# Performance work log

Measured on AMD Instinct MI355X. Metric: run time of the kernel, lower is better.

Reference implementation:

```python
import jax, jax.numpy as jnp
import numpy as np


def _sobel_filters():
    # fil is the 3x3 smoothing kernel [[1,2,1],[2,4,2],[1,2,1]]
    fil = np.array([[1, 2, 1], [2, 4, 2], [1, 2, 1]], dtype=np.float32)
    fx = np.zeros((3, 3, 3), dtype=np.float32)
    fx[0, :, :] = fil
    fx[2, :, :] = -fil
    fy = np.zeros((3, 3, 3), dtype=np.float32)
    fy[:, 0, :] = fil
    fy[:, 2, :] = -fil
    fz = np.zeros((3, 3, 3), dtype=np.float32)
    fz[:, :, 0] = fil
    fz[:, :, 2] = -fil
    # Stack the three fixed (non-learned) filters as 3 output channels: [O=3, I=1, 3,3,3]
    return jnp.asarray(np.stack([fx, fy, fz])[:, None])


_FILT = _sobel_filters()
_DN = ('NCDHW', 'OIDHW', 'NCDHW')


def _grad3d(v):
    # v: [N,1,D,H,W] -> [N,3,D,H,W], padding=1 == SAME for 3x3x3 stride 1
    return jax.lax.conv_general_dilated(
        v, _FILT.astype(v.dtype), window_strides=(1, 1, 1),
        padding='SAME', dimension_numbers=_DN)


def setup_inputs() -> dict:
    key = jax.random.key(0)
    k1, k2 = jax.random.split(key)
    shape = (2, 1, 160, 192, 224)
    x = jax.random.normal(k1, shape, dtype=jnp.float32)
    y = jax.random.normal(k2, shape, dtype=jnp.float32)
    return {"x": x, "y": y}


def reference(x, y):
    gx = _grad3d(x)  # [N,3,D,H,W]
    gy = _grad3d(y)
    d2 = (gx - gy) ** 2
    # sum over the 3 directions of the per-direction MSE
    return jnp.sum(jnp.mean(d2, axis=(0, 2, 3, 4)))
```

## Files before the change

### kernel.cpp

```cpp
#include <hip/hip_runtime.h>


#define N_  2
#define D_  160
#define H_  192
#define W_  224
#define PS  (H_ * W_)

#define TD   8
#define WOUT 62

constexpr float SCALE = 1.0f / ((float)N_ * D_ * H_ * W_);

__global__ __launch_bounds__(256, 6)
void grad_loss_kernel(const float* __restrict__ x, const float* __restrict__ y,
                      float* __restrict__ out) {
    __shared__ float wsum[4];

    const int tid  = threadIdx.x;
    const int lane = tid & 63;
    const int wv   = tid >> 6;

    const int w  = blockIdx.x * WOUT + lane - 1;
    const int h0 = blockIdx.y * 16 + wv * 4;
    const int nchunks = D_ / TD;
    const int nb = blockIdx.z / nchunks;
    const int d0 = (blockIdx.z % nchunks) * TD;

    const bool wok    = (unsigned)w < (unsigned)W_;
    const bool active = (lane >= 1) && (lane <= 62) && wok;

    bool hv[6];
    #pragma unroll
    for (int r = 0; r < 6; ++r)
        hv[r] = (unsigned)(h0 - 1 + r) < (unsigned)H_;

    const float* bx = x + (size_t)nb * D_ * PS;
    const float* by = y + (size_t)nb * D_ * PS;
    const int obase = h0 * W_ + w;

    float a0[4], a1[4], a2[4], b0[4], b1[4], b2[4];
    float vc[6];
    float acc = 0.f;

    {
        const int p = d0 - 1;
        const bool pin = p >= 0;
        #pragma unroll
        for (int r = 0; r < 6; ++r) {
            float xv = 0.f, yv = 0.f;
            if (pin && hv[r] && wok) {
                int o = obase + p * PS + (r - 1) * W_;
                xv = bx[o]; yv = by[o];
            }
            vc[r] = xv - yv;
        }
    }

    #pragma unroll
    for (int it = 0; it <= TD + 1; ++it) {
        float xn[6], yn[6];
        const int p = d0 + it;
        const bool pref = (it <= TD) && (p < D_);
        #pragma unroll
        for (int r = 0; r < 6; ++r) {
            xn[r] = 0.f; yn[r] = 0.f;
            if (pref && hv[r] && wok) {
                int o = obase + p * PS + (r - 1) * W_;
                xn[r] = bx[o]; yn[r] = by[o];
            }
        }

        float sw[6], gw[6];
        #pragma unroll
        for (int r = 0; r < 6; ++r) {
            float L  = __shfl_up(vc[r], 1, 64);
            float Rt = __shfl_down(vc[r], 1, 64);
            sw[r] = (L + Rt) + 2.f * vc[r];
            gw[r] = L - Rt;
        }
        float n0[4], n1[4], n2[4];
        #pragma unroll
        for (int j = 0; j < 4; ++j) {
            n0[j] = sw[j] + 2.f * sw[j + 1] + sw[j + 2];
            n1[j] = sw[j] - sw[j + 2];
            n2[j] = gw[j] + 2.f * gw[j + 1] + gw[j + 2];
        }

        if (it >= 2 && active) {
            #pragma unroll
            for (int j = 0; j < 4; ++j) {
                float gx = a0[j] - n0[j];
                float gy = a1[j] + 2.f * b1[j] + n1[j];
                float gz = a2[j] + 2.f * b2[j] + n2[j];
                acc = fmaf(gx, gx, acc);
                acc = fmaf(gy, gy, acc);
                acc = fmaf(gz, gz, acc);
            }
        }

        #pragma unroll
        for (int j = 0; j < 4; ++j) {
            a0[j] = b0[j]; a1[j] = b1[j]; a2[j] = b2[j];
            b0[j] = n0[j]; b1[j] = n1[j]; b2[j] = n2[j];
        }

        #pragma unroll
        for (int r = 0; r < 6; ++r) vc[r] = xn[r] - yn[r];
    }

    #pragma unroll
    for (int off = 32; off > 0; off >>= 1)
        acc += __shfl_xor(acc, off, 64);
    if (lane == 0) wsum[wv] = acc;
    __syncthreads();
    if (tid == 0) {
        float s = (wsum[0] + wsum[1]) + (wsum[2] + wsum[3]);
        atomicAdd(out, s * SCALE);
    }
}

extern "C" void kernel_launch(void* const* d_in, const int* in_sizes, int n_in,
                              void* d_out, int out_size, void* d_ws, size_t ws_size,
                              hipStream_t stream) {
    const float* x = (const float*)d_in[0];
    const float* y = (const float*)d_in[1];
    float* out = (float*)d_out;

    hipMemsetAsync(out, 0, sizeof(float), stream);

    dim3 block(256);
    dim3 grid((W_ + WOUT - 1) / WOUT,
              H_ / 16,
              N_ * (D_ / TD));
    grad_loss_kernel<<<grid, block, 0, stream>>>(x, y, out);
}
```

Before: 149.6 us.

## Vectorize W with float4 per lane and map one H row per wave

Each lane now handles four consecutive W elements through float4 loads, and one wave covers a full 224-wide row, so there are no overlapping halo columns in W and the grid no longer splits W. Each wave processes one H row and still loads the three neighbouring rows, which raises H-halo reloads from 6/4 to 3/1 per output row. The intent is wider, better-coalesced loads and less wasted work at W tile edges. In exchange, 8 of 64 lanes sit idle, register pressure rises (launch bounds lowered to 4), and traffic from redundant H rows goes up.

```diff
diff --git a/kernel.cpp b/kernel.cpp
--- a/kernel.cpp
+++ b/kernel.cpp
@@ -8,11 +8,10 @@
 #define PS  (H_ * W_)
 
 #define TD   8
-#define WOUT 62
 
 constexpr float SCALE = 1.0f / ((float)N_ * D_ * H_ * W_);
 
-__global__ __launch_bounds__(256, 6)
+__global__ __launch_bounds__(256, 4)
 void grad_loss_kernel(const float* __restrict__ x, const float* __restrict__ y,
                       float* __restrict__ out) {
     __shared__ float wsum[4];
@@ -21,92 +20,110 @@
     const int lane = tid & 63;
     const int wv   = tid >> 6;
 
-    const int w  = blockIdx.x * WOUT + lane - 1;
-    const int h0 = blockIdx.y * 16 + wv * 4;
+    const int h  = blockIdx.y * 4 + wv;
     const int nchunks = D_ / TD;
     const int nb = blockIdx.z / nchunks;
     const int d0 = (blockIdx.z % nchunks) * TD;
 
-    const bool wok    = (unsigned)w < (unsigned)W_;
-    const bool active = (lane >= 1) && (lane <= 62) && wok;
+    const bool wact = lane < 56;
+    const int  w0   = lane * 4;
 
-    bool hv[6];
+    const float* bx = x + (size_t)nb * ((size_t)D_ * PS);
+    const float* by = y + (size_t)nb * ((size_t)D_ * PS);
+
+    bool rok[3];
+    int  ro[3];
     #pragma unroll
-    for (int r = 0; r < 6; ++r)
-        hv[r] = (unsigned)(h0 - 1 + r) < (unsigned)H_;
+    for (int r = 0; r < 3; ++r) {
+        int hr = h - 1 + r;
+        rok[r] = ((unsigned)hr < (unsigned)H_) && wact;
+        ro[r]  = hr * W_ + w0;
+    }
 
-    const float* bx = x + (size_t)nb * D_ * PS;
-    const float* by = y + (size_t)nb * D_ * PS;
-    const int obase = h0 * W_ + w;
-
-    float a0[4], a1[4], a2[4], b0[4], b1[4], b2[4];
-    float vc[6];
+    const float4 z4 = make_float4(0.f, 0.f, 0.f, 0.f);
+    float4 vc[3];
+    float4 a0, a1, a2, b0, b1, b2;
     float acc = 0.f;
 
     {
         const int p = d0 - 1;
         const bool pin = p >= 0;
         #pragma unroll
-        for (int r = 0; r < 6; ++r) {
-            float xv = 0.f, yv = 0.f;
-            if (pin && hv[r] && wok) {
-                int o = obase + p * PS + (r - 1) * W_;
-                xv = bx[o]; yv = by[o];
+        for (int r = 0; r < 3; ++r) {
+            vc[r] = z4;
+            if (pin && rok[r]) {
+                const float4 xv = *(const float4*)(bx + p * PS + ro[r]);
+                const float4 yv = *(const float4*)(by + p * PS + ro[r]);
+                vc[r] = make_float4(xv.x - yv.x, xv.y - yv.y,
+                                    xv.z - yv.z, xv.w - yv.w);
             }
-            vc[r] = xv - yv;
         }
     }
 
     #pragma unroll
     for (int it = 0; it <= TD + 1; ++it) {
-        float xn[6], yn[6];
+        float4 xn[3], yn[3];
         const int p = d0 + it;
         const bool pref = (it <= TD) && (p < D_);
         #pragma unroll
-        for (int r = 0; r < 6; ++r) {
-            xn[r] = 0.f; yn[r] = 0.f;
-            if (pref && hv[r] && wok) {
-                int o = obase + p * PS + (r - 1) * W_;
-                xn[r] = bx[o]; yn[r] = by[o];
+        for (int r = 0; r < 3; ++r) {
+            xn[r] = z4; yn[r] = z4;
+            if (pref && rok[r]) {
+                xn[r] = *(const float4*)(bx + p * PS + ro[r]);
+                yn[r] = *(const float4*)(by + p * PS + ro[r]);
             }
         }
 
-        float sw[6], gw[6];
+        float4 sw[3], gw[3];
         #pragma unroll
-        for (int r = 0; r < 6; ++r) {
-            float L  = __shfl_up(vc[r], 1, 64);
-            float Rt = __shfl_down(vc[r], 1, 64);
-            sw[r] = (L + Rt) + 2.f * vc[r];
-            gw[r] = L - Rt;
+        for (int r = 0; r < 3; ++r) {
+            float Lm = __shfl_up(vc[r].w, 1, 64);
+            float Rp = __shfl_down(vc[r].x, 1, 64);
+            if (lane == 0) Lm = 0.f;
+            const float4 v = vc[r];
+            sw[r] = make_float4(Lm + 2.f * v.x + v.y,
+                                v.x + 2.f * v.y + v.z,
+                                v.y + 2.f * v.z + v.w,
+                                v.z + 2.f * v.w + Rp);
+            gw[r] = make_float4(Lm - v.y, v.x - v.z, v.y - v.w, v.z - Rp);
         }
-        float n0[4], n1[4], n2[4];
-        #pragma unroll
-        for (int j = 0; j < 4; ++j) {
-            n0[j] = sw[j] + 2.f * sw[j + 1] + sw[j + 2];
-            n1[j] = sw[j] - sw[j + 2];
-            n2[j] = gw[j] + 2.f * gw[j + 1] + gw[j + 2];
+        float4 n0 = make_float4(sw[0].x + 2.f * sw[1].x + sw[2].x,
+                                sw[0].y + 2.f * sw[1].y + sw[2].y,
+                                sw[0].z + 2.f * sw[1].z + sw[2].z,
+                                sw[0].w + 2.f * sw[1].w + sw[2].w);
+        float4 n1 = make_float4(sw[0].x - sw[2].x, sw[0].y - sw[2].y,
+                                sw[0].z - sw[2].z, sw[0].w - sw[2].w);
+        float4 n2 = make_float4(gw[0].x + 2.f * gw[1].x + gw[2].x,
+                                gw[0].y + 2.f * gw[1].y + gw[2].y,
+                                gw[0].z + 2.f * gw[1].z + gw[2].z,
+                                gw[0].w + 2.f * gw[1].w + gw[2].w);
+
+        if (it >= 2 && wact) {
+            float4 gx = make_float4(a0.x - n0.x, a0.y - n0.y,
+                                    a0.z - n0.z, a0.w - n0.w);
+            float4 gy = make_float4(a1.x + 2.f * b1.x + n1.x,
+                                    a1.y + 2.f * b1.y + n1.y,
+                                    a1.z + 2.f * b1.z + n1.z,
+                                    a1.w + 2.f * b1.w + n1.w);
+            float4 gz = make_float4(a2.x + 2.f * b2.x + n2.x,
+                                    a2.y + 2.f * b2.y + n2.y,
+                                    a2.z + 2.f * b2.z + n2.z,
+                                    a2.w + 2.f * b2.w + n2.w);
+            acc = fmaf(gx.x, gx.x, acc); acc = fmaf(gx.y, gx.y, acc);
+            acc = fmaf(gx.z, gx.z, acc); acc = fmaf(gx.w, gx.w, acc);
+            acc = fmaf(gy.x, gy.x, acc); acc = fmaf(gy.y, gy.y, acc);
+            acc = fmaf(gy.z, gy.z, acc); acc = fmaf(gy.w, gy.w, acc);
+            acc = fmaf(gz.x, gz.x, acc); acc = fmaf(gz.y, gz.y, acc);
+            acc = fmaf(gz.z, gz.z, acc); acc = fmaf(gz.w, gz.w, acc);
         }
 
-        if (it >= 2 && active) {
-            #pragma unroll
-            for (int j = 0; j < 4; ++j) {
-                float gx = a0[j] - n0[j];
-                float gy = a1[j] + 2.f * b1[j] + n1[j];
-                float gz = a2[j] + 2.f * b2[j] + n2[j];
-                acc = fmaf(gx, gx, acc);
-                acc = fmaf(gy, gy, acc);
-                acc = fmaf(gz, gz, acc);
-            }
-        }
+        a0 = b0; a1 = b1; a2 = b2;
+        b0 = n0; b1 = n1; b2 = n2;
 
         #pragma unroll
-        for (int j = 0; j < 4; ++j) {
-            a0[j] = b0[j]; a1[j] = b1[j]; a2[j] = b2[j];
-            b0[j] = n0[j]; b1[j] = n1[j]; b2[j] = n2[j];
-        }
-
-        #pragma unroll
-        for (int r = 0; r < 6; ++r) vc[r] = xn[r] - yn[r];
+        for (int r = 0; r < 3; ++r)
+            vc[r] = make_float4(xn[r].x - yn[r].x, xn[r].y - yn[r].y,
+                                xn[r].z - yn[r].z, xn[r].w - yn[r].w);
     }
 
     #pragma unroll
@@ -130,8 +147,8 @@
     hipMemsetAsync(out, 0, sizeof(float), stream);
 
     dim3 block(256);
-    dim3 grid((W_ + WOUT - 1) / WOUT,
-              H_ / 16,
+    dim3 grid(1,
+              H_ / 4,
               N_ * (D_ / TD));
     grad_loss_kernel<<<grid, block, 0, stream>>>(x, y, out);
 }
```

Measured after the change: 167.1 us. 1.12x slower.
